# Kernel tuning notes

Hardware: AMD Instinct MI355X
Metric: run time of the kernel (lower is better)

Reference implementation:

```python
import jax, jax.numpy as jnp
import numpy as np

H = 256        # h_dim
H2 = 128       # h_dim // 2
S = 512        # sentence_size
G = 64         # number of component graphs in the batched graph
NN = 100000    # total nodes in batched graph
NE = 200000    # total edges
NENT = 20000   # num entities
NREL = 500     # num relations
B = 32         # batch of query timestamps
SEQ = 10       # seq_len


def setup_inputs() -> dict:
    key = jax.random.key(0)
    ks = jax.random.split(key, 32)
    d = {}
    d["node_ids"] = jax.random.randint(ks[0], (NN,), 0, NENT, dtype=jnp.int32)
    d["edge_src"] = jax.random.randint(ks[1], (NE,), 0, NN, dtype=jnp.int32)
    d["edge_dst"] = jax.random.randint(ks[2], (NE,), 0, NN, dtype=jnp.int32)
    d["edge_type"] = jax.random.randint(ks[3], (NE,), 0, NREL, dtype=jnp.int32)
    d["node2graph"] = jnp.sort(jax.random.randint(ks[4], (NN,), 0, G, dtype=jnp.int32))
    d["edge2graph"] = jnp.sort(jax.random.randint(ks[5], (NE,), 0, G, dtype=jnp.int32))
    d["text_emb"] = jax.random.normal(ks[6], (NE, S), dtype=jnp.float32)
    d["time_idx"] = jax.random.randint(ks[7], (B, SEQ), 0, G, dtype=jnp.int32)
    d["len_non_zero"] = jnp.maximum(jax.random.randint(ks[8], (B,), 0, SEQ, dtype=jnp.int32), 1)
    d["ent_embeds"] = jax.random.normal(ks[9], (NENT, 2 * H), dtype=jnp.float32) * 0.05
    d["ent_memory"] = jax.random.normal(ks[10], (NENT, H), dtype=jnp.float32) * 0.05
    d["rel_embeds"] = jax.random.normal(ks[11], (NREL, 2 * H), dtype=jnp.float32) * 0.05
    d["rel_memory"] = jax.random.normal(ks[12], (NREL, H), dtype=jnp.float32) * 0.05
    sc = lambda k, sh: jax.random.normal(k, sh, dtype=jnp.float32) * (1.0 / np.sqrt(sh[0]))
    d["w_node_W"] = sc(ks[13], (3 * H, H)); d["w_node_b"] = jnp.zeros((H,), jnp.float32)
    d["w_rel_W"] = sc(ks[14], (3 * H, H)); d["w_rel_b"] = jnp.zeros((H,), jnp.float32)
    # CompGCN layer 1: H -> H2 (nodes and edges), text S -> H2
    d["Wn1"] = sc(ks[15], (H, H2)); d["Wl1"] = sc(ks[16], (H, H2))
    d["Wt1"] = sc(ks[17], (S, H2)); d["Wr1"] = sc(ks[18], (H, H2))
    d["b1"] = jnp.zeros((H2,), jnp.float32)
    # CompGCN layer 2: H2 -> H, text S -> H
    d["Wn2"] = sc(ks[19], (H2, H)); d["Wl2"] = sc(ks[20], (H2, H))
    d["Wt2"] = sc(ks[21], (S, H)); d["Wr2"] = sc(ks[22], (H2, H))
    d["b2"] = jnp.zeros((H,), jnp.float32)
    return d


def _compgcn_layer(h, e, text, src, dst, Wn, Wl, Wt, Wr, b, n_nodes):
    # composition = subtraction: msg = (h_src - e_h) @ Wn + text @ Wt
    msg = (h[src] - e) @ Wn + text @ Wt                      # [NE, out]
    agg = jax.ops.segment_sum(msg, dst, num_segments=n_nodes)
    deg = jax.ops.segment_sum(jnp.ones((msg.shape[0],), msg.dtype), dst, num_segments=n_nodes)
    agg = agg / jnp.maximum(deg, 1.0)[:, None]
    h_new = jax.nn.relu(agg + h @ Wl + b)                    # self-loop + bias + relu
    e_new = jax.nn.relu(e @ Wr)                              # relation transform
    return h_new, e_new


def reference(node_ids, edge_src, edge_dst, edge_type, node2graph, edge2graph,
              text_emb, time_idx, len_non_zero,
              ent_embeds, ent_memory, rel_embeds, rel_memory,
              w_node_W, w_node_b, w_rel_W, w_rel_b,
              Wn1, Wl1, Wt1, Wr1, b1, Wn2, Wl2, Wt2, Wr2, b2):
    n_nodes = node_ids.shape[0]
    # initial node / edge features: cat(embed[2h], memory[h]) -> Linear(3h, h)
    h = jnp.concatenate([ent_embeds[node_ids], ent_memory[node_ids]], axis=1) @ w_node_W + w_node_b
    e = jnp.concatenate([rel_embeds[edge_type], rel_memory[edge_type]], axis=1) @ w_rel_W + w_rel_b
    # two CompGCN relational message-passing layers: H -> H2 -> H
    h, e = _compgcn_layer(h, e, text_emb, edge_src, edge_dst, Wn1, Wl1, Wt1, Wr1, b1, n_nodes)
    h, e = _compgcn_layer(h, e, text_emb, edge_src, edge_dst, Wn2, Wl2, Wt2, Wr2, b2, n_nodes)
    # dgl.max_nodes / dgl.max_edges: per-graph max pooling (maxpool == 1)
    gn = jax.ops.segment_max(h, node2graph, num_segments=G)   # [G, H]
    ge = jax.ops.segment_max(e, edge2graph, num_segments=G)   # [G, H]
    global_info = jnp.concatenate([gn, ge], axis=-1)          # [G, 2H]
    # ragged temporal gather: embed_seq[i, j] = global_info[time_to_idx[time_list[i][j]]]
    seq = global_info[time_idx]                               # [B, SEQ, 2H]
    mask = (jnp.arange(SEQ, dtype=jnp.int32)[None, :] < len_non_zero[:, None])
    seq = seq * mask[..., None].astype(seq.dtype)             # zeros past len_non_zero
    # dropout at eval time is identity
    return seq, len_non_zero
```

## Files before the change

### kernel.cpp

```cpp
#include <hip/hip_runtime.h>

#define HD    256
#define HD2   128
#define SDIM  512
#define GNUM  64
#define NN    100000
#define NE    200000
#define NENT  20000
#define NREL  500
#define BNUM  32
#define SEQL  10

typedef __attribute__((ext_vector_type(4))) float f32x4;
typedef __attribute__((ext_vector_type(8))) short bf16x8;

__device__ __forceinline__ short to_bf(float f) {
    unsigned u = __float_as_uint(f);
    u += 0x7fff + ((u >> 16) & 1);
    return (short)(u >> 16);
}
__device__ __forceinline__ float bf_to_f(unsigned short u) {
    return __uint_as_float(((unsigned)u) << 16);
}


__global__ void k_cnt(const int* __restrict__ edst, int* __restrict__ cnt) {
    int e = blockIdx.x * 256 + threadIdx.x;
    if (e < NE) atomicAdd(&cnt[edst[e]], 1);
}

__global__ void k_scan_blk(const int* __restrict__ cnt, int* __restrict__ row_off,
                           int* __restrict__ bsum) {
    __shared__ int s[256];
    int i = blockIdx.x * 256 + threadIdx.x;
    int v = cnt[i];
    s[threadIdx.x] = v;
    __syncthreads();
    for (int d = 1; d < 256; d <<= 1) {
        int t = (threadIdx.x >= d) ? s[threadIdx.x - d] : 0;
        __syncthreads();
        s[threadIdx.x] += t;
        __syncthreads();
    }
    row_off[i] = s[threadIdx.x] - v;
    if (threadIdx.x == 255) bsum[blockIdx.x] = s[255];
}

__global__ void k_scan_top(int* __restrict__ bsum) {
    __shared__ int s[512];
    int v = (threadIdx.x < 391) ? bsum[threadIdx.x] : 0;
    s[threadIdx.x] = v;
    __syncthreads();
    for (int d = 1; d < 512; d <<= 1) {
        int t = (threadIdx.x >= d) ? s[threadIdx.x - d] : 0;
        __syncthreads();
        s[threadIdx.x] += t;
        __syncthreads();
    }
    if (threadIdx.x < 391) bsum[threadIdx.x] = s[threadIdx.x] - v;
}

__global__ void k_scan_add(int* __restrict__ row_off, const int* __restrict__ bsum,
                           int* __restrict__ cur) {
    int i = blockIdx.x * 256 + threadIdx.x;
    int v = row_off[i] + bsum[blockIdx.x];
    row_off[i] = v;
    cur[i] = v;
}

__global__ void k_fill(const int* __restrict__ edst, const int* __restrict__ esrc,
                       const int* __restrict__ etype, const int* __restrict__ node_ids,
                       int* __restrict__ cur, int* __restrict__ eidx,
                       int* __restrict__ esrcC, int* __restrict__ etC,
                       int* __restrict__ nidC) {
    int e = blockIdx.x * 256 + threadIdx.x;
    if (e < NE) {
        int pos = atomicAdd(&cur[edst[e]], 1);
        int s = esrc[e];
        eidx[pos] = e;
        esrcC[pos] = s;
        etC[pos] = etype[e];
        nidC[pos] = node_ids[s];
    }
}


__global__ void k_rel_feat(const float* __restrict__ rel_emb, const float* __restrict__ rel_mem,
                           const float* __restrict__ W, const float* __restrict__ b,
                           float* __restrict__ rel_feat) {
    __shared__ float s[768];
    int r = blockIdx.x, j = threadIdx.x;
    for (int k = j; k < 768; k += 256)
        s[k] = (k < 512) ? rel_emb[r * 512 + k] : rel_mem[r * 256 + (k - 512)];
    __syncthreads();
    float acc = b[j];
    for (int k = 0; k < 768; ++k) acc += s[k] * W[k * 256 + j];
    rel_feat[r * 256 + j] = acc;
}

__global__ void k_rel_l1(const float* __restrict__ rel_feat, const float* __restrict__ Wn1,
                         const float* __restrict__ Wr1, float* __restrict__ ecomb,
                         float* __restrict__ er1) {
    __shared__ float s[256];
    int r = blockIdx.x, j = threadIdx.x;
    s[j] = rel_feat[r * 256 + j];
    __syncthreads();
    if (j < 128) {
        float acc = 0.f;
        for (int k = 0; k < 256; ++k) acc += s[k] * Wn1[k * 128 + j];
        ecomb[r * 384 + j] = acc;
    } else {
        int jj = j - 128;
        float acc = 0.f;
        for (int k = 0; k < 256; ++k) acc += s[k] * Wr1[k * 128 + jj];
        er1[r * 128 + jj] = fmaxf(acc, 0.f);
    }
}

__global__ void k_rel_l2(const float* __restrict__ er1, const float* __restrict__ Wr2,
                         const float* __restrict__ Wn2, float* __restrict__ er2,
                         float* __restrict__ ecomb) {
    __shared__ float s[128];
    int r = blockIdx.x, j = threadIdx.x;
    if (j < 128) s[j] = er1[r * 128 + j];
    __syncthreads();
    float a = 0.f, c = 0.f;
    for (int k = 0; k < 128; ++k) {
        float v = s[k];
        a += v * Wr2[k * 256 + j];
        c += v * Wn2[k * 256 + j];
    }
    er2[r * 256 + j] = fmaxf(a, 0.f);
    ecomb[r * 384 + 128 + j] = c;
}


__global__ void k_cw(const float* __restrict__ wnW, const float* __restrict__ Wn1,
                     const float* __restrict__ Wl1, float* __restrict__ cw) {
    __shared__ float s[256];
    int k = blockIdx.x, j = threadIdx.x;
    s[j] = wnW[k * 256 + j];
    __syncthreads();
    float acc = 0.f;
    if (j < 128) {
        for (int m = 0; m < 256; ++m) acc += s[m] * Wn1[m * 128 + j];
    } else {
        int jj = j - 128;
        for (int m = 0; m < 256; ++m) acc += s[m] * Wl1[m * 128 + jj];
    }
    cw[k * 256 + j] = acc;
}

__global__ void k_cb(const float* __restrict__ wnb, const float* __restrict__ Wn1,
                     const float* __restrict__ Wl1, float* __restrict__ bc) {
    int j = threadIdx.x;
    float acc = 0.f;
    if (j < 128) {
        for (int m = 0; m < 256; ++m) acc += wnb[m] * Wn1[m * 128 + j];
    } else {
        int jj = j - 128;
        for (int m = 0; m < 256; ++m) acc += wnb[m] * Wl1[m * 128 + jj];
    }
    bc[j] = acc;
}

__global__ void k_pack(const float* __restrict__ src, bf16x8* __restrict__ dst,
                       int K, int N) {
    int KF = K >> 5;
    int fid = blockIdx.x;
    int n = fid / KF, kk = fid - n * KF;
    int lane = threadIdx.x;
    int col = n * 16 + (lane & 15);
    int kb = kk * 32 + (lane >> 4) * 8;
    bf16x8 v;
#pragma unroll
    for (int j = 0; j < 8; ++j) v[j] = to_bf(src[(size_t)(kb + j) * N + col]);
    dst[(size_t)fid * 64 + lane] = v;
}


__global__ void __launch_bounds__(256) k_ent(const float* __restrict__ ee,
                                             const float* __restrict__ em,
                                             const bf16x8* __restrict__ cwf,
                                             const float* __restrict__ bc,
                                             float* __restrict__ ha1,
                                             float* __restrict__ hb1) {
    __shared__ bf16x8 sA[2048];
    int tid = threadIdx.x;
    int e0 = blockIdx.x * 64;
    int wave = tid >> 6, lane = tid & 63;
    int gs = (tid >> 4) & 3, rs = tid & 15;
    int rowS = ((tid >> 6) & 3) * 16 + rs;
    int ent = e0 + rowS;
    if (ent >= NENT) ent = NENT - 1;
    f32x4 acc[4][4];
#pragma unroll
    for (int mf = 0; mf < 4; ++mf)
#pragma unroll
        for (int nf = 0; nf < 4; ++nf) acc[mf][nf] = (f32x4)0.f;

    for (int ch = 0; ch < 3; ++ch) {
        if (ch) __syncthreads();
#pragma unroll
        for (int it = 0; it < 8; ++it) {
            int gc = ch * 256 + it * 32 + gs * 8;
            const float4* p = (gc < 512)
                ? (const float4*)(ee + (size_t)ent * 512 + gc)
                : (const float4*)(em + (size_t)ent * 256 + (gc - 512));
            float4 x = p[0], y = p[1];
            bf16x8 v;
            v[0] = to_bf(x.x); v[1] = to_bf(x.y); v[2] = to_bf(x.z); v[3] = to_bf(x.w);
            v[4] = to_bf(y.x); v[5] = to_bf(y.y); v[6] = to_bf(y.z); v[7] = to_bf(y.w);
            sA[it * 256 + tid] = v;
        }
        __syncthreads();
#pragma unroll
        for (int kkl = 0; kkl < 8; ++kkl) {
            bf16x8 a[4], b[4];
#pragma unroll
            for (int mf = 0; mf < 4; ++mf) a[mf] = sA[kkl * 256 + mf * 64 + lane];
#pragma unroll
            for (int nf = 0; nf < 4; ++nf)
                b[nf] = cwf[(size_t)((wave * 4 + nf) * 24 + ch * 8 + kkl) * 64 + lane];
#pragma unroll
            for (int mf = 0; mf < 4; ++mf)
#pragma unroll
                for (int nf = 0; nf < 4; ++nf)
                    acc[mf][nf] = __builtin_amdgcn_mfma_f32_16x16x32_bf16(a[mf], b[nf],
                                                                          acc[mf][nf], 0, 0, 0);
        }
    }
    int gq = lane >> 4, cl = lane & 15;
#pragma unroll
    for (int mf = 0; mf < 4; ++mf)
#pragma unroll
        for (int nf = 0; nf < 4; ++nf) {
            int c = wave * 64 + nf * 16 + cl;
            float bb = bc[c];
#pragma unroll
            for (int q = 0; q < 4; ++q) {
                int m = e0 + mf * 16 + gq * 4 + q;
                if (m < NENT) {
                    float val = acc[mf][nf][q] + bb;
                    if (c < 128) ha1[(size_t)m * 128 + c] = val;
                    else hb1[(size_t)m * 128 + (c - 128)] = val;
                }
            }
        }
}


__global__ void __launch_bounds__(256, 2) k_edge(const float* __restrict__ text,
                                                 const bf16x8* __restrict__ wtf,
                                                 unsigned short* __restrict__ msg) {
    __shared__ bf16x8 sA[4096];
    int tid = threadIdx.x;
    size_t e0 = (size_t)blockIdx.x * 64;
    int R = ((tid >> 6) << 4) + (tid & 15);
    int g = (tid >> 4) & 3;
    const float* trow = text + (e0 + R) * 512 + g * 8;

    float4 xv[16], yv[16];
#pragma unroll
    for (int kk = 0; kk < 16; ++kk) {
        const float4* p = (const float4*)(trow + kk * 32);
        xv[kk] = p[0];
        yv[kk] = p[1];
    }
#pragma unroll
    for (int kk = 0; kk < 16; ++kk) {
        bf16x8 v;
        v[0] = to_bf(xv[kk].x); v[1] = to_bf(xv[kk].y);
        v[2] = to_bf(xv[kk].z); v[3] = to_bf(xv[kk].w);
        v[4] = to_bf(yv[kk].x); v[5] = to_bf(yv[kk].y);
        v[6] = to_bf(yv[kk].z); v[7] = to_bf(yv[kk].w);
        sA[kk * 256 + tid] = v;
    }
    __syncthreads();

    int wave = tid >> 6, lane = tid & 63;
    f32x4 acc[4][6];
#pragma unroll
    for (int mf = 0; mf < 4; ++mf)
#pragma unroll
        for (int nf = 0; nf < 6; ++nf) acc[mf][nf] = (f32x4)0.f;

#pragma unroll
    for (int kk = 0; kk < 16; ++kk) {
        bf16x8 a[4], b[6];
#pragma unroll
        for (int mf = 0; mf < 4; ++mf) a[mf] = sA[kk * 256 + mf * 64 + lane];
#pragma unroll
        for (int nf = 0; nf < 6; ++nf)
            b[nf] = wtf[(size_t)((wave * 6 + nf) * 16 + kk) * 64 + lane];
#pragma unroll
        for (int mf = 0; mf < 4; ++mf)
#pragma unroll
            for (int nf = 0; nf < 6; ++nf)
                acc[mf][nf] = __builtin_amdgcn_mfma_f32_16x16x32_bf16(a[mf], b[nf],
                                                                      acc[mf][nf], 0, 0, 0);
    }

    int gq = lane >> 4, cl = lane & 15;
#pragma unroll
    for (int mf = 0; mf < 4; ++mf)
#pragma unroll
        for (int nf = 0; nf < 6; ++nf) {
            int c = wave * 96 + nf * 16 + cl;
            f32x4 v = acc[mf][nf];
#pragma unroll
            for (int q = 0; q < 4; ++q) {
                int row = mf * 16 + gq * 4 + q;
                msg[(e0 + row) * 384 + c] = (unsigned short)to_bf(v[q]);
            }
        }
}


__global__ void __launch_bounds__(256) k_agg(const unsigned short* __restrict__ msg,
                                             const int* __restrict__ row_off,
                                             const int* __restrict__ eidx,
                                             const int* __restrict__ etC,
                                             const int* __restrict__ nidC,
                                             const int* __restrict__ node_ids,
                                             const float* __restrict__ ha1,
                                             const float* __restrict__ ecomb,
                                             const float* __restrict__ hb1,
                                             const float* __restrict__ b1,
                                             unsigned short* __restrict__ h1b,
                                             unsigned short* __restrict__ agg2b) {
    int n = blockIdx.x * 4 + (threadIdx.x >> 6);
    int lane = threadIdx.x & 63;
    if (n >= NN) return;
    int beg = row_off[n], end = row_off[n + 1];
    float d = fmaxf((float)(end - beg), 1.f);
    int nid0 = node_ids[n];
    int c = lane * 2;
    float a0 = 0.f, a1 = 0.f, a2 = 0.f, a3 = 0.f, a4 = 0.f, a5 = 0.f;
    const unsigned* m32 = (const unsigned*)msg;
    for (int i = beg; i < end; ++i) {
        size_t e = (size_t)eidx[i];
        int et = etC[i], nid = nidC[i];
        size_t base = e * 192;
        unsigned u0 = m32[base + lane];
        unsigned u1 = m32[base + 64 + lane];
        unsigned u2 = m32[base + 128 + lane];
        const float2 ec0 = *(const float2*)(ecomb + (size_t)et * 384 + c);
        const float2 ec1 = *(const float2*)(ecomb + (size_t)et * 384 + 128 + c);
        const float2 ec2 = *(const float2*)(ecomb + (size_t)et * 384 + 256 + c);
        const float2 hv = *(const float2*)(ha1 + (size_t)nid * 128 + c);
        a0 += bf_to_f((unsigned short)(u0 & 0xffff)) + hv.x - ec0.x;
        a1 += bf_to_f((unsigned short)(u0 >> 16)) + hv.y - ec0.y;
        a2 += bf_to_f((unsigned short)(u1 & 0xffff)) - ec1.x;
        a3 += bf_to_f((unsigned short)(u1 >> 16)) - ec1.y;
        a4 += bf_to_f((unsigned short)(u2 & 0xffff)) - ec2.x;
        a5 += bf_to_f((unsigned short)(u2 >> 16)) - ec2.y;
    }
    const float2 hb = *(const float2*)(hb1 + (size_t)nid0 * 128 + c);
    const float2 bb = *(const float2*)(b1 + c);
    float hx = fmaxf(a0 / d + hb.x + bb.x, 0.f);
    float hy = fmaxf(a1 / d + hb.y + bb.y, 0.f);
    unsigned hp = ((unsigned)(unsigned short)to_bf(hx)) |
                  (((unsigned)(unsigned short)to_bf(hy)) << 16);
    ((unsigned*)h1b)[(size_t)n * 64 + lane] = hp;
    unsigned g0 = ((unsigned)(unsigned short)to_bf(a2)) |
                  (((unsigned)(unsigned short)to_bf(a3)) << 16);
    unsigned g1 = ((unsigned)(unsigned short)to_bf(a4)) |
                  (((unsigned)(unsigned short)to_bf(a5)) << 16);
    ((unsigned*)agg2b)[(size_t)n * 128 + lane] = g0;
    ((unsigned*)agg2b)[(size_t)n * 128 + 64 + lane] = g1;
}


__global__ void __launch_bounds__(256) k_s1(const unsigned short* __restrict__ h1b,
                                            const int* __restrict__ row_off,
                                            const int* __restrict__ esrcC,
                                            float* __restrict__ s1) {
    int n = blockIdx.x * 4 + (threadIdx.x >> 6);
    int lane = threadIdx.x & 63;
    if (n >= NN) return;
    int beg = row_off[n], end = row_off[n + 1];
    float2 acc; acc.x = 0.f; acc.y = 0.f;
    const unsigned* h32 = (const unsigned*)h1b;
    for (int i = beg; i < end; ++i) {
        int src = esrcC[i];
        unsigned u = h32[(size_t)src * 64 + lane];
        acc.x += bf_to_f((unsigned short)(u & 0xffff));
        acc.y += bf_to_f((unsigned short)(u >> 16));
    }
    ((float2*)(s1 + (size_t)n * 128))[lane] = acc;
}


__global__ void __launch_bounds__(256) k_h2(const float* __restrict__ s1,
                                            const unsigned short* __restrict__ h1b,
                                            const unsigned short* __restrict__ agg2b,
                                            const int* __restrict__ cnt,
                                            const int* __restrict__ n2g,
                                            const bf16x8* __restrict__ wn2f,
                                            const bf16x8* __restrict__ wl2f,
                                            const float* __restrict__ b2,
                                            float* __restrict__ gn) {
    __shared__ bf16x8 sS[1024], sH[1024];
    __shared__ int s_g[64];
    int tid = threadIdx.x, n0 = blockIdx.x * 64;
    int wave = tid >> 6, lane = tid & 63;
    if (tid < 64) {
        int m = n0 + tid;
        if (m >= NN) m = NN - 1;
        s_g[tid] = n2g[m];
    }
    {
        int gsv = (tid >> 4) & 3, rsv = tid & 15;
        int row = ((tid >> 6) & 3) * 16 + rsv;
        int m = n0 + row;
        if (m >= NN) m = NN - 1;
#pragma unroll
        for (int kk = 0; kk < 4; ++kk) {
            int cb = kk * 32 + gsv * 8;
            const float4* ps = (const float4*)(s1 + (size_t)m * 128 + cb);
            float4 sx = ps[0], sy = ps[1];
            bf16x8 vs;
            vs[0] = to_bf(sx.x); vs[1] = to_bf(sx.y); vs[2] = to_bf(sx.z); vs[3] = to_bf(sx.w);
            vs[4] = to_bf(sy.x); vs[5] = to_bf(sy.y); vs[6] = to_bf(sy.z); vs[7] = to_bf(sy.w);
            bf16x8 vh = *(const bf16x8*)(h1b + (size_t)m * 128 + cb);
            sS[kk * 256 + tid] = vs;
            sH[kk * 256 + tid] = vh;
        }
    }
    __syncthreads();
    f32x4 aa[4][4], ab[4][4];
#pragma unroll
    for (int mf = 0; mf < 4; ++mf)
#pragma unroll
        for (int nf = 0; nf < 4; ++nf) { aa[mf][nf] = (f32x4)0.f; ab[mf][nf] = (f32x4)0.f; }
#pragma unroll
    for (int kk = 0; kk < 4; ++kk) {
        bf16x8 a1[4], a2[4], bv1[4], bv2[4];
#pragma unroll
        for (int mf = 0; mf < 4; ++mf) {
            a1[mf] = sS[kk * 256 + mf * 64 + lane];
            a2[mf] = sH[kk * 256 + mf * 64 + lane];
        }
#pragma unroll
        for (int nf = 0; nf < 4; ++nf) {
            bv1[nf] = wn2f[(size_t)((wave * 4 + nf) * 4 + kk) * 64 + lane];
            bv2[nf] = wl2f[(size_t)((wave * 4 + nf) * 4 + kk) * 64 + lane];
        }
#pragma unroll
        for (int mf = 0; mf < 4; ++mf)
#pragma unroll
            for (int nf = 0; nf < 4; ++nf) {
                aa[mf][nf] = __builtin_amdgcn_mfma_f32_16x16x32_bf16(a1[mf], bv1[nf],
                                                                     aa[mf][nf], 0, 0, 0);
                ab[mf][nf] = __builtin_amdgcn_mfma_f32_16x16x32_bf16(a2[mf], bv2[nf],
                                                                     ab[mf][nf], 0, 0, 0);
            }
    }
    int gq = lane >> 4, cl = lane & 15;
    float dinv[4][4];
#pragma unroll
    for (int mf = 0; mf < 4; ++mf)
#pragma unroll
        for (int q = 0; q < 4; ++q) {
            int m = n0 + mf * 16 + gq * 4 + q;
            if (m >= NN) m = NN - 1;
            dinv[mf][q] = 1.f / fmaxf((float)cnt[m], 1.f);
        }
    float b2v[4];
#pragma unroll
    for (int nf = 0; nf < 4; ++nf) b2v[nf] = b2[wave * 64 + nf * 16 + cl];
#pragma unroll
    for (int mf = 0; mf < 4; ++mf)
#pragma unroll
        for (int nf = 0; nf < 4; ++nf) {
            int c = wave * 64 + nf * 16 + cl;
#pragma unroll
            for (int q = 0; q < 4; ++q) {
                int m = n0 + mf * 16 + gq * 4 + q;
                if (m >= NN) m = NN - 1;
                float araw = bf_to_f(agg2b[(size_t)m * 256 + c]);
                aa[mf][nf][q] = fmaxf((araw + aa[mf][nf][q]) * dinv[mf][q]
                                      + ab[mf][nf][q] + b2v[nf], 0.f);
            }
        }
    int g0 = s_g[0], g63 = s_g[63];
    if (g0 == g63) {
#pragma unroll
        for (int nf = 0; nf < 4; ++nf) {
            float mx = 0.f;
#pragma unroll
            for (int mf = 0; mf < 4; ++mf)
#pragma unroll
                for (int q = 0; q < 4; ++q) mx = fmaxf(mx, aa[mf][nf][q]);
            mx = fmaxf(mx, __shfl_xor(mx, 16));
            mx = fmaxf(mx, __shfl_xor(mx, 32));
            if (gq == 0) {
                int c = wave * 64 + nf * 16 + cl;
                atomicMax((int*)&gn[(size_t)g0 * 256 + c], __float_as_int(mx));
            }
        }
    } else {
#pragma unroll
        for (int mf = 0; mf < 4; ++mf)
#pragma unroll
            for (int q = 0; q < 4; ++q) {
                int row = mf * 16 + gq * 4 + q;
                int m = n0 + row;
                if (m >= NN) continue;
                int gg = s_g[row];
#pragma unroll
                for (int nf = 0; nf < 4; ++nf) {
                    int c = wave * 64 + nf * 16 + cl;
                    atomicMax((int*)&gn[(size_t)gg * 256 + c],
                              __float_as_int(aa[mf][nf][q]));
                }
            }
    }
}


__device__ __forceinline__ int lower_bound_i(const int* __restrict__ a, int n, int v) {
    int lo = 0, hi = n;
    while (lo < hi) {
        int m = (lo + hi) >> 1;
        if (a[m] < v) lo = m + 1; else hi = m;
    }
    return lo;
}

__global__ void k_gmax_edges(const float* __restrict__ er2, const int* __restrict__ e2g,
                             const int* __restrict__ etype, float* __restrict__ ge) {
    int g = blockIdx.x, q = blockIdx.y, j = threadIdx.x;
    int lo = lower_bound_i(e2g, NE, g);
    int hi = lower_bound_i(e2g, NE, g + 1);
    float mx = 0.f;
    for (int e = lo + q; e < hi; e += 16) mx = fmaxf(mx, er2[etype[e] * 256 + j]);
    atomicMax((int*)&ge[g * 256 + j], __float_as_int(mx));
}

__global__ void k_out(const float* __restrict__ gn, const float* __restrict__ ge,
                      const int* __restrict__ time_idx, const int* __restrict__ lens,
                      float* __restrict__ out) {
    int idx = blockIdx.x * 256 + threadIdx.x;
    const int NOUT = BNUM * SEQL * 512;
    if (idx < NOUT) {
        int j = idx & 511;
        int bt = idx >> 9;
        int b = bt / SEQL, t = bt - b * SEQL;
        float v = 0.f;
        if (t < lens[b]) {
            int g = time_idx[bt];
            v = (j < 256) ? gn[g * 256 + j] : ge[g * 256 + (j - 256)];
        }
        out[idx] = v;
    } else if (idx < NOUT + BNUM) {
        int b = idx - NOUT;
        out[idx] = (float)lens[b];
    }
}


extern "C" void kernel_launch(void* const* d_in, const int* in_sizes, int n_in,
                              void* d_out, int out_size, void* d_ws, size_t ws_size,
                              hipStream_t stream) {
    const int*   node_ids  = (const int*)d_in[0];
    const int*   edge_src  = (const int*)d_in[1];
    const int*   edge_dst  = (const int*)d_in[2];
    const int*   edge_type = (const int*)d_in[3];
    const int*   node2g    = (const int*)d_in[4];
    const int*   edge2g    = (const int*)d_in[5];
    const float* text_emb  = (const float*)d_in[6];
    const int*   time_idx  = (const int*)d_in[7];
    const int*   lens      = (const int*)d_in[8];
    const float* ent_emb   = (const float*)d_in[9];
    const float* ent_mem   = (const float*)d_in[10];
    const float* rel_emb   = (const float*)d_in[11];
    const float* rel_mem   = (const float*)d_in[12];
    const float* w_node_W  = (const float*)d_in[13];
    const float* w_node_b  = (const float*)d_in[14];
    const float* w_rel_W   = (const float*)d_in[15];
    const float* w_rel_b   = (const float*)d_in[16];
    const float* Wn1 = (const float*)d_in[17];
    const float* Wl1 = (const float*)d_in[18];
    const float* Wt1 = (const float*)d_in[19];
    const float* Wr1 = (const float*)d_in[20];
    const float* b1  = (const float*)d_in[21];
    const float* Wn2 = (const float*)d_in[22];
    const float* Wl2 = (const float*)d_in[23];
    const float* Wt2 = (const float*)d_in[24];
    const float* Wr2 = (const float*)d_in[25];
    const float* b2  = (const float*)d_in[26];

    float* ws = (float*)d_ws;
    size_t off = 0;
    float* rel_feat = ws + off; off += (size_t)NREL * 256;
    float* er1      = ws + off; off += (size_t)NREL * 128;
    float* er2      = ws + off; off += (size_t)NREL * 256;
    float* ecomb    = ws + off; off += (size_t)NREL * 384;
    float* ha1      = ws + off; off += (size_t)NENT * 128;
    float* hb1      = ws + off; off += (size_t)NENT * 128;
    float* cw       = ws + off; off += (size_t)768 * 256;
    float* bc       = ws + off; off += 256;
    bf16x8* wtf  = (bf16x8*)(ws + off); off += (size_t)24 * 16 * 64 * 4;
    bf16x8* cwf  = (bf16x8*)(ws + off); off += (size_t)16 * 24 * 64 * 4;
    bf16x8* wn2f = (bf16x8*)(ws + off); off += (size_t)16 * 4 * 64 * 4;
    bf16x8* wl2f = (bf16x8*)(ws + off); off += (size_t)16 * 4 * 64 * 4;
    int*   cnt = (int*)(ws + off);
    size_t zoff = off;          off += 100096;
    float* gn  = ws + off;      off += (size_t)GNUM * 256;
    float* ge  = ws + off;      off += (size_t)GNUM * 256;
    size_t zbytes = (off - zoff) * sizeof(float);
    int* row_off = (int*)(ws + off); off += 100352;
    int* cur     = (int*)(ws + off); off += 100096;
    int* bsum    = (int*)(ws + off); off += 512;
    int* eidx    = (int*)(ws + off); off += (size_t)NE;
    int* esrcC   = (int*)(ws + off); off += (size_t)NE;
    int* etC     = (int*)(ws + off); off += (size_t)NE;
    int* nidC    = (int*)(ws + off); off += (size_t)NE;
    unsigned short* msg = (unsigned short*)(ws + off);
    float* s1 = ws + off;
    off += (size_t)NE * 384 / 2;
    unsigned short* h1b   = (unsigned short*)(ws + off); off += (size_t)NN * 64;
    unsigned short* agg2b = (unsigned short*)(ws + off); off += (size_t)NN * 128;

    hipMemsetAsync((void*)cnt, 0, zbytes, stream);

    k_cnt<<<(NE + 255) / 256, 256, 0, stream>>>(edge_dst, cnt);
    k_scan_blk<<<391, 256, 0, stream>>>(cnt, row_off, bsum);
    k_scan_top<<<1, 512, 0, stream>>>(bsum);
    k_scan_add<<<391, 256, 0, stream>>>(row_off, bsum, cur);
    k_fill<<<(NE + 255) / 256, 256, 0, stream>>>(edge_dst, edge_src, edge_type, node_ids,
                                                 cur, eidx, esrcC, etC, nidC);

    k_rel_feat<<<NREL, 256, 0, stream>>>(rel_emb, rel_mem, w_rel_W, w_rel_b, rel_feat);
    k_rel_l1<<<NREL, 256, 0, stream>>>(rel_feat, Wn1, Wr1, ecomb, er1);
    k_rel_l2<<<NREL, 256, 0, stream>>>(er1, Wr2, Wn2, er2, ecomb);

    k_cw<<<768, 256, 0, stream>>>(w_node_W, Wn1, Wl1, cw);
    k_cb<<<1, 256, 0, stream>>>(w_node_b, Wn1, Wl1, bc);
    k_pack<<<8 * 16, 64, 0, stream>>>(Wt1, wtf, 512, 128);
    k_pack<<<16 * 16, 64, 0, stream>>>(Wt2, wtf + (size_t)8 * 16 * 64, 512, 256);
    k_pack<<<16 * 24, 64, 0, stream>>>(cw, cwf, 768, 256);
    k_pack<<<16 * 4, 64, 0, stream>>>(Wn2, wn2f, 128, 256);
    k_pack<<<16 * 4, 64, 0, stream>>>(Wl2, wl2f, 128, 256);

    k_ent<<<(NENT + 63) / 64, 256, 0, stream>>>(ent_emb, ent_mem, cwf, bc, ha1, hb1);

    k_edge<<<NE / 64, 256, 0, stream>>>(text_emb, wtf, msg);

    k_agg<<<NN / 4, 256, 0, stream>>>(msg, row_off, eidx, etC, nidC, node_ids,
                                      ha1, ecomb, hb1, b1, h1b, agg2b);
    k_s1<<<NN / 4, 256, 0, stream>>>(h1b, row_off, esrcC, s1);
    k_h2<<<(NN + 63) / 64, 256, 0, stream>>>(s1, h1b, agg2b, cnt, node2g,
                                             wn2f, wl2f, b2, gn);

    k_gmax_edges<<<dim3(GNUM, 16), 256, 0, stream>>>(er2, edge2g, edge_type, ge);
    k_out<<<(BNUM * SEQL * 512 + BNUM + 255) / 256, 256, 0, stream>>>(gn, ge, time_idx, lens,
                                                                      (float*)d_out);
}
```

Before: 581.2 us.

## Write edge messages in CSR order, halve edge LDS tile, store s1 as bf16

k_fill now records each edge's CSR position (an inverse permutation) instead of the edge index. k_edge scatters its message rows directly to that sorted slot, so k_agg reads messages contiguously with no eidx indirection. k_edge also stages the text tile in two K halves, halving LDS and raising the occupancy hint from 2 to 3 blocks. k_s1 stores its sums packed as bf16, so k_h2 loads them without converting. The costs are scattered row writes in k_edge, an extra barrier, and rounding s1 to bf16 earlier than before.

```diff
diff --git a/kernel.cpp b/kernel.cpp
--- a/kernel.cpp
+++ b/kernel.cpp
@@ -70,14 +70,14 @@
 
 __global__ void k_fill(const int* __restrict__ edst, const int* __restrict__ esrc,
                        const int* __restrict__ etype, const int* __restrict__ node_ids,
-                       int* __restrict__ cur, int* __restrict__ eidx,
+                       int* __restrict__ cur, int* __restrict__ pinv,
                        int* __restrict__ esrcC, int* __restrict__ etC,
                        int* __restrict__ nidC) {
     int e = blockIdx.x * 256 + threadIdx.x;
     if (e < NE) {
         int pos = atomicAdd(&cur[edst[e]], 1);
         int s = esrc[e];
-        eidx[pos] = e;
+        pinv[e] = pos;
         esrcC[pos] = s;
         etC[pos] = etype[e];
         nidC[pos] = node_ids[s];
@@ -250,34 +250,19 @@
 }
 
 
-__global__ void __launch_bounds__(256, 2) k_edge(const float* __restrict__ text,
+__global__ void __launch_bounds__(256, 3) k_edge(const float* __restrict__ text,
+                                                 const int* __restrict__ pinv,
                                                  const bf16x8* __restrict__ wtf,
                                                  unsigned short* __restrict__ msg) {
-    __shared__ bf16x8 sA[4096];
+    __shared__ bf16x8 sA[2048];
+    __shared__ int s_pos[64];
     int tid = threadIdx.x;
     size_t e0 = (size_t)blockIdx.x * 64;
+    if (tid < 64) s_pos[tid] = pinv[e0 + tid];
     int R = ((tid >> 6) << 4) + (tid & 15);
     int g = (tid >> 4) & 3;
     const float* trow = text + (e0 + R) * 512 + g * 8;
 
-    float4 xv[16], yv[16];
-#pragma unroll
-    for (int kk = 0; kk < 16; ++kk) {
-        const float4* p = (const float4*)(trow + kk * 32);
-        xv[kk] = p[0];
-        yv[kk] = p[1];
-    }
-#pragma unroll
-    for (int kk = 0; kk < 16; ++kk) {
-        bf16x8 v;
-        v[0] = to_bf(xv[kk].x); v[1] = to_bf(xv[kk].y);
-        v[2] = to_bf(xv[kk].z); v[3] = to_bf(xv[kk].w);
-        v[4] = to_bf(yv[kk].x); v[5] = to_bf(yv[kk].y);
-        v[6] = to_bf(yv[kk].z); v[7] = to_bf(yv[kk].w);
-        sA[kk * 256 + tid] = v;
-    }
-    __syncthreads();
-
     int wave = tid >> 6, lane = tid & 63;
     f32x4 acc[4][6];
 #pragma unroll
@@ -286,19 +271,43 @@
         for (int nf = 0; nf < 6; ++nf) acc[mf][nf] = (f32x4)0.f;
 
 #pragma unroll
-    for (int kk = 0; kk < 16; ++kk) {
-        bf16x8 a[4], b[6];
-#pragma unroll
-        for (int mf = 0; mf < 4; ++mf) a[mf] = sA[kk * 256 + mf * 64 + lane];
-#pragma unroll
-        for (int nf = 0; nf < 6; ++nf)
-            b[nf] = wtf[(size_t)((wave * 6 + nf) * 16 + kk) * 64 + lane];
-#pragma unroll
-        for (int mf = 0; mf < 4; ++mf)
+    for (int p = 0; p < 2; ++p) {
+        if (p) __syncthreads();
+#pragma unroll
+        for (int h = 0; h < 2; ++h) {
+            float4 xs[4], ys[4];
+#pragma unroll
+            for (int k2 = 0; k2 < 4; ++k2) {
+                const float4* p4 = (const float4*)(trow + p * 256 + (h * 4 + k2) * 32);
+                xs[k2] = p4[0];
+                ys[k2] = p4[1];
+            }
+#pragma unroll
+            for (int k2 = 0; k2 < 4; ++k2) {
+                bf16x8 v;
+                v[0] = to_bf(xs[k2].x); v[1] = to_bf(xs[k2].y);
+                v[2] = to_bf(xs[k2].z); v[3] = to_bf(xs[k2].w);
+                v[4] = to_bf(ys[k2].x); v[5] = to_bf(ys[k2].y);
+                v[6] = to_bf(ys[k2].z); v[7] = to_bf(ys[k2].w);
+                sA[(h * 4 + k2) * 256 + tid] = v;
+            }
+        }
+        __syncthreads();
+#pragma unroll
+        for (int kkl = 0; kkl < 8; ++kkl) {
+            bf16x8 a[4], b[6];
+#pragma unroll
+            for (int mf = 0; mf < 4; ++mf) a[mf] = sA[kkl * 256 + mf * 64 + lane];
 #pragma unroll
             for (int nf = 0; nf < 6; ++nf)
-                acc[mf][nf] = __builtin_amdgcn_mfma_f32_16x16x32_bf16(a[mf], b[nf],
-                                                                      acc[mf][nf], 0, 0, 0);
+                b[nf] = wtf[(size_t)((wave * 6 + nf) * 16 + p * 8 + kkl) * 64 + lane];
+#pragma unroll
+            for (int mf = 0; mf < 4; ++mf)
+#pragma unroll
+                for (int nf = 0; nf < 6; ++nf)
+                    acc[mf][nf] = __builtin_amdgcn_mfma_f32_16x16x32_bf16(a[mf], b[nf],
+                                                                          acc[mf][nf], 0, 0, 0);
+        }
     }
 
     int gq = lane >> 4, cl = lane & 15;
@@ -311,7 +320,7 @@
 #pragma unroll
             for (int q = 0; q < 4; ++q) {
                 int row = mf * 16 + gq * 4 + q;
-                msg[(e0 + row) * 384 + c] = (unsigned short)to_bf(v[q]);
+                msg[(size_t)s_pos[row] * 384 + c] = (unsigned short)to_bf(v[q]);
             }
         }
 }
@@ -319,7 +328,6 @@
 
 __global__ void __launch_bounds__(256) k_agg(const unsigned short* __restrict__ msg,
                                              const int* __restrict__ row_off,
-                                             const int* __restrict__ eidx,
                                              const int* __restrict__ etC,
                                              const int* __restrict__ nidC,
                                              const int* __restrict__ node_ids,
@@ -339,9 +347,8 @@
     float a0 = 0.f, a1 = 0.f, a2 = 0.f, a3 = 0.f, a4 = 0.f, a5 = 0.f;
     const unsigned* m32 = (const unsigned*)msg;
     for (int i = beg; i < end; ++i) {
-        size_t e = (size_t)eidx[i];
         int et = etC[i], nid = nidC[i];
-        size_t base = e * 192;
+        size_t base = (size_t)i * 192;
         unsigned u0 = m32[base + lane];
         unsigned u1 = m32[base + 64 + lane];
         unsigned u2 = m32[base + 128 + lane];
@@ -375,24 +382,26 @@
 __global__ void __launch_bounds__(256) k_s1(const unsigned short* __restrict__ h1b,
                                             const int* __restrict__ row_off,
                                             const int* __restrict__ esrcC,
-                                            float* __restrict__ s1) {
+                                            unsigned short* __restrict__ s1b) {
     int n = blockIdx.x * 4 + (threadIdx.x >> 6);
     int lane = threadIdx.x & 63;
     if (n >= NN) return;
     int beg = row_off[n], end = row_off[n + 1];
-    float2 acc; acc.x = 0.f; acc.y = 0.f;
+    float ax = 0.f, ay = 0.f;
     const unsigned* h32 = (const unsigned*)h1b;
     for (int i = beg; i < end; ++i) {
         int src = esrcC[i];
         unsigned u = h32[(size_t)src * 64 + lane];
-        acc.x += bf_to_f((unsigned short)(u & 0xffff));
-        acc.y += bf_to_f((unsigned short)(u >> 16));
-    }
-    ((float2*)(s1 + (size_t)n * 128))[lane] = acc;
-}
-
-
-__global__ void __launch_bounds__(256) k_h2(const float* __restrict__ s1,
+        ax += bf_to_f((unsigned short)(u & 0xffff));
+        ay += bf_to_f((unsigned short)(u >> 16));
+    }
+    unsigned p = ((unsigned)(unsigned short)to_bf(ax)) |
+                 (((unsigned)(unsigned short)to_bf(ay)) << 16);
+    ((unsigned*)s1b)[(size_t)n * 64 + lane] = p;
+}
+
+
+__global__ void __launch_bounds__(256) k_h2(const unsigned short* __restrict__ s1b,
                                             const unsigned short* __restrict__ h1b,
                                             const unsigned short* __restrict__ agg2b,
                                             const int* __restrict__ cnt,
@@ -418,14 +427,8 @@
 #pragma unroll
         for (int kk = 0; kk < 4; ++kk) {
             int cb = kk * 32 + gsv * 8;
-            const float4* ps = (const float4*)(s1 + (size_t)m * 128 + cb);
-            float4 sx = ps[0], sy = ps[1];
-            bf16x8 vs;
-            vs[0] = to_bf(sx.x); vs[1] = to_bf(sx.y); vs[2] = to_bf(sx.z); vs[3] = to_bf(sx.w);
-            vs[4] = to_bf(sy.x); vs[5] = to_bf(sy.y); vs[6] = to_bf(sy.z); vs[7] = to_bf(sy.w);
-            bf16x8 vh = *(const bf16x8*)(h1b + (size_t)m * 128 + cb);
-            sS[kk * 256 + tid] = vs;
-            sH[kk * 256 + tid] = vh;
+            sS[kk * 256 + tid] = *(const bf16x8*)(s1b + (size_t)m * 128 + cb);
+            sH[kk * 256 + tid] = *(const bf16x8*)(h1b + (size_t)m * 128 + cb);
         }
     }
     __syncthreads();
@@ -614,12 +617,12 @@
     int* row_off = (int*)(ws + off); off += 100352;
     int* cur     = (int*)(ws + off); off += 100096;
     int* bsum    = (int*)(ws + off); off += 512;
-    int* eidx    = (int*)(ws + off); off += (size_t)NE;
+    int* pinv    = (int*)(ws + off); off += (size_t)NE;
     int* esrcC   = (int*)(ws + off); off += (size_t)NE;
     int* etC     = (int*)(ws + off); off += (size_t)NE;
     int* nidC    = (int*)(ws + off); off += (size_t)NE;
     unsigned short* msg = (unsigned short*)(ws + off);
-    float* s1 = ws + off;
+    unsigned short* s1b = (unsigned short*)(ws + off);
     off += (size_t)NE * 384 / 2;
     unsigned short* h1b   = (unsigned short*)(ws + off); off += (size_t)NN * 64;
     unsigned short* agg2b = (unsigned short*)(ws + off); off += (size_t)NN * 128;
@@ -631,7 +634,7 @@
     k_scan_top<<<1, 512, 0, stream>>>(bsum);
     k_scan_add<<<391, 256, 0, stream>>>(row_off, bsum, cur);
     k_fill<<<(NE + 255) / 256, 256, 0, stream>>>(edge_dst, edge_src, edge_type, node_ids,
-                                                 cur, eidx, esrcC, etC, nidC);
+                                                 cur, pinv, esrcC, etC, nidC);
 
     k_rel_feat<<<NREL, 256, 0, stream>>>(rel_emb, rel_mem, w_rel_W, w_rel_b, rel_feat);
     k_rel_l1<<<NREL, 256, 0, stream>>>(rel_feat, Wn1, Wr1, ecomb, er1);
@@ -647,12 +650,12 @@
 
     k_ent<<<(NENT + 63) / 64, 256, 0, stream>>>(ent_emb, ent_mem, cwf, bc, ha1, hb1);
 
-    k_edge<<<NE / 64, 256, 0, stream>>>(text_emb, wtf, msg);
-
-    k_agg<<<NN / 4, 256, 0, stream>>>(msg, row_off, eidx, etC, nidC, node_ids,
+    k_edge<<<NE / 64, 256, 0, stream>>>(text_emb, pinv, wtf, msg);
+
+    k_agg<<<NN / 4, 256, 0, stream>>>(msg, row_off, etC, nidC, node_ids,
                                       ha1, ecomb, hb1, b1, h1b, agg2b);
-    k_s1<<<NN / 4, 256, 0, stream>>>(h1b, row_off, esrcC, s1);
-    k_h2<<<(NN + 63) / 64, 256, 0, stream>>>(s1, h1b, agg2b, cnt, node2g,
+    k_s1<<<NN / 4, 256, 0, stream>>>(h1b, row_off, esrcC, s1b);
+    k_h2<<<(NN + 63) / 64, 256, 0, stream>>>(s1b, h1b, agg2b, cnt, node2g,
                                              wn2f, wl2f, b2, gn);
 
     k_gmax_edges<<<dim3(GNUM, 16), 256, 0, stream>>>(er2, edge2g, edge_type, ge);
```

New measurement: 580.9 us (median of 2 runs). No clear change (-0.1%).
